# Kernel tuning notes

Hardware: AMD Instinct MI355X
Metric: run time of the kernel (lower is better)

The kernel has to match this reference:

```python
import jax, jax.numpy as jnp
import numpy as np

N_TYPES = 6
NUM_HEADS = 8
MAX_SEQ = 50
LN_EPS = 1e-5
NEG_SLOPE = 0.2


def layer_norm(x, g, b):
    m = x.mean(-1, keepdims=True)
    v = ((x - m) ** 2).mean(-1, keepdims=True)
    return (x - m) / jnp.sqrt(v + LN_EPS) * g + b


def setup_inputs() -> dict:
    key = jax.random.key(0)
    N, E, D = 20000, 200000, 128  # nodes, edges, input_dim==hidden_dim
    ks = jax.random.split(key, 64)
    it = iter(ks)

    def w(shape):
        return jax.random.normal(next(it), shape, jnp.float32) / np.sqrt(shape[-2] if len(shape) > 1 else shape[-1]).astype(np.float32)

    inp = {}
    inp['x'] = jax.random.normal(next(it), (N, D), jnp.float32)
    inp['edge_index'] = jax.random.randint(next(it), (2, E), 0, N)
    inp['node_types'] = jax.random.randint(next(it), (N,), 0, N_TYPES)
    inp['temporal_positions'] = jax.random.randint(next(it), (N,), 0, MAX_SEQ)
    # CrossDomainGAT params
    inp['gat_Wq'] = w((D, D)); inp['gat_Wk'] = w((D, D)); inp['gat_Wv'] = w((D, D))
    inp['gat_Wo'] = w((D, D)); inp['gat_bo'] = jnp.zeros((D,), jnp.float32)
    inp['gat_g'] = jnp.ones((D,), jnp.float32); inp['gat_b'] = jnp.zeros((D,), jnp.float32)
    # SchemaAwareGCN params
    inp['gcn_Wt'] = w((N_TYPES, D, D)); inp['gcn_bt'] = jnp.zeros((N_TYPES, D), jnp.float32)
    inp['gcn_mW1'] = w((2 * D, D)); inp['gcn_mb1'] = jnp.zeros((D,), jnp.float32)
    inp['gcn_mW2'] = w((D, D)); inp['gcn_mb2'] = jnp.zeros((D,), jnp.float32)
    inp['gcn_aW1'] = w((D, D)); inp['gcn_ab1'] = jnp.zeros((D,), jnp.float32)
    inp['gcn_aW2'] = w((D, D)); inp['gcn_ab2'] = jnp.zeros((D,), jnp.float32)
    inp['gcn_Wo'] = w((D, D)); inp['gcn_bo'] = jnp.zeros((D,), jnp.float32)
    inp['gcn_g'] = jnp.ones((D,), jnp.float32); inp['gcn_b'] = jnp.zeros((D,), jnp.float32)
    # TemporalReasoningGNN params (no turn_boundaries -> LSTM/attention path skipped)
    inp['tmp_emb'] = jax.random.normal(next(it), (MAX_SEQ, D), jnp.float32)
    inp['tmp_W1'] = w((2 * D, D)); inp['tmp_b1'] = jnp.zeros((D,), jnp.float32)
    inp['tmp_W2'] = w((D, D)); inp['tmp_b2'] = jnp.zeros((D,), jnp.float32)
    inp['tmp_Wo'] = w((D, D)); inp['tmp_bo'] = jnp.zeros((D,), jnp.float32)
    inp['tmp_g'] = jnp.ones((D,), jnp.float32); inp['tmp_b'] = jnp.zeros((D,), jnp.float32)
    # Unified fusion (concat of 3 branches -> hidden) + LayerNorm
    inp['fus_W'] = w((3 * D, D)); inp['fus_b'] = jnp.zeros((D,), jnp.float32)
    inp['fus_g'] = jnp.ones((D,), jnp.float32); inp['fus_be'] = jnp.zeros((D,), jnp.float32)
    return inp


def _gat(x, row, col, Wq, Wk, Wv, Wo, bo, g, b):
    N, D = x.shape
    Dh = D // NUM_HEADS
    Q = (x @ Wq).reshape(N, NUM_HEADS, Dh)
    K = (x @ Wk).reshape(N, NUM_HEADS, Dh)
    V = (x @ Wv).reshape(N, NUM_HEADS, Dh)
    # edge-wise multi-head attention scores [E, H]
    scores = (Q[row] * K[col]).sum(-1) / np.sqrt(Dh).astype(np.float32)
    scores = jax.nn.leaky_relu(scores, NEG_SLOPE)
    # segment softmax over incoming edges of each col node
    mx = jax.ops.segment_max(scores, col, num_segments=N)
    ex = jnp.exp(scores - mx[col])
    sm = jax.ops.segment_sum(ex, col, num_segments=N)
    probs = ex / sm[col]
    wv = probs[:, :, None] * V[row]  # [E, H, Dh]
    out = jax.ops.segment_sum(wv.reshape(len(row), D), col, num_segments=N)
    out = out @ Wo + bo
    return layer_norm(out + x, g, b)


def _mlp2(z, W1, b1, W2, b2):
    return jax.nn.relu(z @ W1 + b1) @ W2 + b2


def _gcn(x, row, col, node_types, Wt, bt, mW1, mb1, mW2, mb2, aW1, ab1, aW2, ab2, Wo, bo, g, b):
    N, D = x.shape
    h = jnp.zeros((N, D), x.dtype)
    for t in range(N_TYPES):  # fixed small type count
        h = h + jnp.where((node_types == t)[:, None], x @ Wt[t] + bt[t], 0.0)
    messages = _mlp2(jnp.concatenate([h[row], h[col]], axis=1), mW1, mb1, mW2, mb2)
    agg = jax.ops.segment_sum(messages, col, num_segments=N)
    h = h + _mlp2(agg, aW1, ab1, aW2, ab2)
    h = h @ Wo + bo
    return layer_norm(h + x, g, b)


def _temporal(x, row, col, tpos, emb, W1, b1, W2, b2, Wo, bo, g, b):
    N, D = x.shape
    h = x + emb[jnp.clip(tpos, 0, MAX_SEQ - 1)]
    messages = _mlp2(jnp.concatenate([h[row], h[col]], axis=1), W1, b1, W2, b2)
    h = h + jax.ops.segment_sum(messages, col, num_segments=N)
    h = h @ Wo + bo
    return layer_norm(h, g, b)


def reference(x, edge_index, node_types, temporal_positions,
              gat_Wq, gat_Wk, gat_Wv, gat_Wo, gat_bo, gat_g, gat_b,
              gcn_Wt, gcn_bt, gcn_mW1, gcn_mb1, gcn_mW2, gcn_mb2,
              gcn_aW1, gcn_ab1, gcn_aW2, gcn_ab2, gcn_Wo, gcn_bo, gcn_g, gcn_b,
              tmp_emb, tmp_W1, tmp_b1, tmp_W2, tmp_b2, tmp_Wo, tmp_bo, tmp_g, tmp_b,
              fus_W, fus_b, fus_g, fus_be):
    row, col = edge_index[0], edge_index[1]
    o_gat = _gat(x, row, col, gat_Wq, gat_Wk, gat_Wv, gat_Wo, gat_bo, gat_g, gat_b)
    o_gcn = _gcn(x, row, col, node_types, gcn_Wt, gcn_bt, gcn_mW1, gcn_mb1, gcn_mW2, gcn_mb2,
                 gcn_aW1, gcn_ab1, gcn_aW2, gcn_ab2, gcn_Wo, gcn_bo, gcn_g, gcn_b)
    o_tmp = _temporal(x, row, col, temporal_positions, tmp_emb, tmp_W1, tmp_b1, tmp_W2, tmp_b2,
                      tmp_Wo, tmp_bo, tmp_g, tmp_b)
    fused = jnp.concatenate([o_gat, o_gcn, o_tmp], axis=-1) @ fus_W + fus_b
    return layer_norm(fused, fus_g, fus_be)
```

## Files before the change

kernel.cpp:

```cpp
#include <hip/hip_runtime.h>

using u32 = unsigned int;
using s64 = long long;

__global__ __launch_bounds__(64) void k_detect13(const u32* __restrict__ ei,
                                                 const u32* __restrict__ nt,
                                                 const u32* __restrict__ tp,
                                                 u32* __restrict__ flags) {
    if (blockIdx.x != 0 || threadIdx.x != 0) return;
    bool e64 = true, n64 = true, t64 = true;
    for (int k = 0; k < 64; ++k) {
        if (ei[2 * k + 1] != 0u) e64 = false;
        if (nt[2 * k + 1] != 0u) n64 = false;
        if (tp[2 * k + 1] != 0u) t64 = false;
    }
    flags[0] = e64 ? 1u : 0u;
    flags[1] = n64 ? 1u : 0u;
    flags[2] = t64 ? 1u : 0u;
}

__global__ __launch_bounds__(256) void k_cvt13(const void* __restrict__ src,
                                               int* __restrict__ dst, long long n,
                                               const u32* __restrict__ flags, int fidx) {
    long long i = (long long)blockIdx.x * 256 + threadIdx.x;
// ... 179 lines not shown
    int t = threadIdx.x;
#pragma unroll
    for (int ii = 0; ii < 4; ++ii) {
        int idx = t + ii * 256;
        int r = idx >> 5, c = idx & 31;
        int node = i0 + r; if (node >= N) node = N - 1;
        st4(xs + r * 128 + c * 4, ld4(src + (size_t)node * 128 + c * 4));
    }
}

__device__ __forceinline__ void xstore(float* xs, const float4 (&v)[4], int tn, int tc) {
#pragma unroll
    for (int j = 0; j < 4; ++j) st4(xs + (tn * 4 + j) * 128 + tc * 4, v[j]);
}

__global__ __launch_bounds__(256) void k_qkvT(const float* __restrict__ x,
                                              const float* __restrict__ Wq,
                                              const float* __restrict__ Wk,
                                              const float* __restrict__ Wv,
                                              float* __restrict__ big, int N) {
    __shared__ float xs[32 * 128];
    __shared__ float wl[64 * 128];
    int t = threadIdx.x, tn = t >> 5, tc = t & 31;
    int i0 = blockIdx.x * 32;
    stage32(xs, x, i0, N);
    float4 acc[4];
    const float* Ws[3] = {Wq, Wk, Wv};
#pragma unroll
    for (int m = 0; m < 3; ++m) {
#pragma unroll
        for (int j = 0; j < 4; ++j) acc[j] = make_float4(0.f, 0.f, 0.f, 0.f);
        mmS(acc, xs, wl, Ws[m], tn, tc);
#pragma unroll
        for (int j = 0; j < 4; ++j) {
            int node = i0 + tn * 4 + j;
            if (node < N) st4(big + (size_t)node * 384 + m * 128 + tc * 4, acc[j]);
        }
    }
}

__global__ __launch_bounds__(256) void k_gat_smB(const float* __restrict__ big,
                                                 const int* __restrict__ ei, int E,
                                                 float* __restrict__ scores,
                                                 float* __restrict__ sm) {
    long long t = (long long)blockIdx.x * 256 + threadIdx.x;
    if (t >= (long long)E * 8) return;
    int e = (int)(t >> 3), h = (int)(t & 7);
    int row = ei[e], col = ei[E + e];
    const float4* q = (const float4*)(big + (size_t)row * 384 + h * 16);
    const float4* kk = (const float4*)(big + (size_t)col * 384 + 128 + h * 16);
    float s = 0.f;
#pragma unroll
    for (int d = 0; d < 4; ++d) {
        float4 a = q[d], b = kk[d];
        s += a.x * b.x + a.y * b.y + a.z * b.z + a.w * b.w;
    }
    s *= 0.25f;
    s = s > 0.f ? s : 0.2f * s;
    float ex = expf(s);
    scores[t] = ex;
    atomicAdd(&sm[(size_t)col * 8 + h], ex);
}

__global__ __launch_bounds__(256) void k_wvS2(const float* __restrict__ big,
                                              const float* __restrict__ scores,
                                              const float* __restrict__ sm,
                                              const int* __restrict__ srow,
                                              const int* __restrict__ sedge,
                                              const int* __restrict__ offA,
                                              float* __restrict__ agg, int N) {
    int l = threadIdx.x & 63;
    int col = blockIdx.x * 4 + (threadIdx.x >> 6);
    if (col >= N) return;
    int h = l >> 3;
    float sv = sm[(size_t)col * 8 + h];
    float ism = sv != 0.f ? 1.f / sv : 0.f;
// ... 5 lines not shown
        float pr1 = scores[(size_t)e1 * 8 + h] * ism;
        float2 v0 = ld2(big + (size_t)r0 * 384 + 256 + 2 * l);
        float2 v1 = ld2(big + (size_t)r1 * 384 + 256 + 2 * l);
        ax = fmaf(pr0, v0.x, ax); ay = fmaf(pr0, v0.y, ay);
        ax = fmaf(pr1, v1.x, ax); ay = fmaf(pr1, v1.y, ay);
    }
    for (; p < pe; ++p) {
        int e = sedge[p], r = srow[p];
        float pr = scores[(size_t)e * 8 + h] * ism;
        float2 v = ld2(big + (size_t)r * 384 + 256 + 2 * l);
        ax = fmaf(pr, v.x, ax); ay = fmaf(pr, v.y, ay);
    }
    st2(agg + (size_t)col * 128 + 2 * l, make_float2(ax, ay));
}

__global__ __launch_bounds__(256) void k_ep_gatT(const float* __restrict__ x,
                                                 const float* __restrict__ agg,
                                                 const float* __restrict__ Wo,
                                                 const float* __restrict__ bo,
                                                 const float* __restrict__ g,
                                                 const float* __restrict__ b,
                                                 const float* __restrict__ fusW,
                                                 const float* __restrict__ fus_b,
                                                 float* __restrict__ fused, int N) {
    __shared__ float xs[32 * 128];
    __shared__ float wl[64 * 128];
    int t = threadIdx.x, tn = t >> 5, tc = t & 31;
    int i0 = blockIdx.x * 32;
    stage32(xs, agg, i0, N);
    float4 acc[4];
    float4 bo4 = ld4(bo + tc * 4);
#pragma unroll
    for (int j = 0; j < 4; ++j) acc[j] = bo4;
    mmS(acc, xs, wl, Wo, tn, tc);
    float4 o[4];
#pragma unroll
    for (int j = 0; j < 4; ++j) {
        int node = i0 + tn * 4 + j; if (node >= N) node = N - 1;
        float4 xr = ld4(x + (size_t)node * 128 + tc * 4);
        float4 v = make_float4(acc[j].x + xr.x, acc[j].y + xr.y,
                               acc[j].z + xr.z, acc[j].w + xr.w);
        o[j] = lnrow(v, g, b, tc);
    }
    __syncthreads();
    xstore(xs, o, tn, tc);
    float4 fb4 = ld4(fus_b + tc * 4);
#pragma unroll
    for (int j = 0; j < 4; ++j) acc[j] = fb4;
    mmS(acc, xs, wl, fusW, tn, tc);
#pragma unroll
    for (int j = 0; j < 4; ++j) {
        int node = i0 + tn * 4 + j;
        if (node < N) st4(fused + (size_t)node * 128 + tc * 4, acc[j]);
    }
}

__global__ __launch_bounds__(256) void k_hgcnT(const float* __restrict__ x,
                                               const int* __restrict__ nt,
                                               const int* __restrict__ perm,
                                               const float* __restrict__ Wt,
                                               const float* __restrict__ bt,
                                               float* __restrict__ h_gcn, int N) {
    __shared__ float xs[32 * 128];
    __shared__ float wl[64 * 128];
    int t = threadIdx.x, tn = t >> 5, tc = t & 31;
    int i0 = blockIdx.x * 32;
#pragma unroll
    for (int ii = 0; ii < 4; ++ii) {
        int idx = t + ii * 256;
        int r = idx >> 5, c = idx & 31;
        int q = i0 + r; if (q >= N) q = N - 1;
        int node = perm[q];
        st4(xs + r * 128 + c * 4, ld4(x + (size_t)node * 128 + c * 4));
    }
    int qa = i0; if (qa >= N) qa = N - 1;
    int qb = i0 + 31; if (qb >= N) qb = N - 1;
    int t0 = nt[perm[qa]]; t0 = (t0 < 0 || t0 > 5) ? 0 : t0;
    int t1 = nt[perm[qb]]; t1 = (t1 < 0 || t1 > 5) ? 0 : t1;
    float4 acc[4];
    if (t0 == t1) {
#pragma unroll
        for (int j = 0; j < 4; ++j) acc[j] = ld4(bt + t0 * 128 + tc * 4);
        mmS(acc, xs, wl, Wt + (size_t)t0 * 16384, tn, tc);
    } else {
        __syncthreads();
#pragma unroll
        for (int j = 0; j < 4; ++j) {
            int q = i0 + tn * 4 + j; if (q >= N) q = N - 1;
            int tt = nt[perm[q]]; tt = (tt < 0 || tt > 5) ? 0 : tt;
            const float* W = Wt + (size_t)tt * 16384;
            float4 a = ld4(bt + tt * 128 + tc * 4);
#pragma unroll 2
            for (int k4 = 0; k4 < 32; ++k4) {
                float4 xv = ld4(xs + (tn * 4 + j) * 128 + k4 * 4);
                float4 w0 = ld4(W + (size_t)(k4 * 4 + 0) * 128 + tc * 4);
                float4 w1 = ld4(W + (size_t)(k4 * 4 + 1) * 128 + tc * 4);
                float4 w2 = ld4(W + (size_t)(k4 * 4 + 2) * 128 + tc * 4);
                float4 w3 = ld4(W + (size_t)(k4 * 4 + 3) * 128 + tc * 4);
                fma4(a, xv.x, w0); fma4(a, xv.y, w1);
                fma4(a, xv.z, w2); fma4(a, xv.w, w3);
            }
            acc[j] = a;
        }
    }
#pragma unroll
    for (int j = 0; j < 4; ++j) {
        int q = i0 + tn * 4 + j;
        if (q < N) st4(h_gcn + (size_t)perm[q] * 128 + tc * 4, acc[j]);
    }
}

__global__ __launch_bounds__(256) void k_preT(const float* __restrict__ h,
                                              const float* __restrict__ emb,
                                              const int* __restrict__ tpos,
                                              const float* __restrict__ W1,
                                              const float* __restrict__ b1,
                                              float* __restrict__ Pa,
                                              float* __restrict__ Pb, int N, int mode) {
    __shared__ float xs[32 * 128];
    __shared__ float wl[64 * 128];
    int t = threadIdx.x, tn = t >> 5, tc = t & 31;
    int i0 = blockIdx.x * 32;
#pragma unroll
    for (int ii = 0; ii < 4; ++ii) {
        int idx = t + ii * 256;
        int r = idx >> 5, c = idx & 31;
        int node = i0 + r; if (node >= N) node = N - 1;
        float4 v = ld4(h + (size_t)node * 128 + c * 4);
        if (mode) {
            int tp = tpos[node]; tp = tp < 0 ? 0 : (tp > 49 ? 49 : tp);
            float4 e = ld4(emb + tp * 128 + c * 4);
            v.x += e.x; v.y += e.y; v.z += e.z; v.w += e.w;
        }
        st4(xs + r * 128 + c * 4, v);
    }
    float4 acc[4];
#pragma unroll
    for (int j = 0; j < 4; ++j) acc[j] = make_float4(0.f, 0.f, 0.f, 0.f);
    mmS(acc, xs, wl, W1, tn, tc);
#pragma unroll
    for (int j = 0; j < 4; ++j) {
        int node = i0 + tn * 4 + j;
        if (node < N) st4(Pa + (size_t)node * 128 + tc * 4, acc[j]);
    }
    float4 b14 = ld4(b1 + tc * 4);
#pragma unroll
    for (int j = 0; j < 4; ++j) acc[j] = b14;
    mmS(acc, xs, wl, W1 + (size_t)128 * 128, tn, tc);
#pragma unroll
    for (int j = 0; j < 4; ++j) {
        int node = i0 + tn * 4 + j;
        if (node < N) st4(Pb + (size_t)node * 128 + tc * 4, acc[j]);
    }
}

__global__ __launch_bounds__(256) void k_rsum2(const float* __restrict__ Pa,
                                               const float* __restrict__ Pb,
                                               const int* __restrict__ srow,
                                               const int* __restrict__ offA,
                                               float* __restrict__ s, int N) {
    int l = threadIdx.x & 63;
    int col = blockIdx.x * 4 + (threadIdx.x >> 6);
    if (col >= N) return;
    float2 pb = ld2(Pb + (size_t)col * 128 + 2 * l);
    float ax = 0.f, ay = 0.f;
    int p = offA[col], pe = offA[col + 1];
    for (; p + 4 <= pe; p += 4) {
        int r0 = srow[p], r1 = srow[p + 1], r2 = srow[p + 2], r3 = srow[p + 3];
        float2 a0 = ld2(Pa + (size_t)r0 * 128 + 2 * l);
        float2 a1 = ld2(Pa + (size_t)r1 * 128 + 2 * l);
        float2 a2 = ld2(Pa + (size_t)r2 * 128 + 2 * l);
        float2 a3 = ld2(Pa + (size_t)r3 * 128 + 2 * l);
        ax += fmaxf(a0.x + pb.x, 0.f) + fmaxf(a1.x + pb.x, 0.f)
            + fmaxf(a2.x + pb.x, 0.f) + fmaxf(a3.x + pb.x, 0.f);
        ay += fmaxf(a0.y + pb.y, 0.f) + fmaxf(a1.y + pb.y, 0.f)
            + fmaxf(a2.y + pb.y, 0.f) + fmaxf(a3.y + pb.y, 0.f);
    }
    for (; p < pe; ++p) {
        int r = srow[p];
        float2 a = ld2(Pa + (size_t)r * 128 + 2 * l);
        ax += fmaxf(a.x + pb.x, 0.f);
        ay += fmaxf(a.y + pb.y, 0.f);
    }
    st2(s + (size_t)col * 128 + 2 * l, make_float2(ax, ay));
}

__global__ __launch_bounds__(256) void k_ep_gcnT(const float* __restrict__ x,
                                                 const float* __restrict__ h_gcn,
                                                 const float* __restrict__ s,
                                                 const int* __restrict__ offA,
                                                 const float* __restrict__ W2,
                                                 const float* __restrict__ b2,
                                                 const float* __restrict__ aW1,
                                                 const float* __restrict__ ab1,
                                                 const float* __restrict__ aW2,
                                                 const float* __restrict__ ab2,
                                                 const float* __restrict__ Wo,
                                                 const float* __restrict__ bo,
                                                 const float* __restrict__ g,
                                                 const float* __restrict__ b,
                                                 const float* __restrict__ fusW,
                                                 float* __restrict__ fused, int N) {
    __shared__ float xs[32 * 128];
    __shared__ float wl[64 * 128];
    int t = threadIdx.x, tn = t >> 5, tc = t & 31;
    int i0 = blockIdx.x * 32;
    int node[4];
#pragma unroll
    for (int j = 0; j < 4; ++j) {
        node[j] = i0 + tn * 4 + j; if (node[j] >= N) node[j] = N - 1;
    }
    stage32(xs, s, i0, N);
    float4 acc[4];
    float4 b24 = ld4(b2 + tc * 4);
#pragma unroll
    for (int j = 0; j < 4; ++j) {
        float deg = (float)(offA[node[j] + 1] - offA[node[j]]);
        acc[j] = make_float4(deg * b24.x, deg * b24.y, deg * b24.z, deg * b24.w);
    }
    mmS(acc, xs, wl, W2, tn, tc);
    __syncthreads();
    xstore(xs, acc, tn, tc);
    float4 a14 = ld4(ab1 + tc * 4);
#pragma unroll
    for (int j = 0; j < 4; ++j) acc[j] = a14;
    mmS(acc, xs, wl, aW1, tn, tc);
#pragma unroll
    for (int j = 0; j < 4; ++j) {
        acc[j].x = fmaxf(acc[j].x, 0.f); acc[j].y = fmaxf(acc[j].y, 0.f);
        acc[j].z = fmaxf(acc[j].z, 0.f); acc[j].w = fmaxf(acc[j].w, 0.f);
    }
    __syncthreads();
    xstore(xs, acc, tn, tc);
    float4 a24 = ld4(ab2 + tc * 4);
#pragma unroll
    for (int j = 0; j < 4; ++j) acc[j] = a24;
    mmS(acc, xs, wl, aW2, tn, tc);
#pragma unroll
    for (int j = 0; j < 4; ++j) {
        float4 hg = ld4(h_gcn + (size_t)node[j] * 128 + tc * 4);
        acc[j].x += hg.x; acc[j].y += hg.y; acc[j].z += hg.z; acc[j].w += hg.w;
    }
    __syncthreads();
    xstore(xs, acc, tn, tc);
    float4 bo4 = ld4(bo + tc * 4);
#pragma unroll
    for (int j = 0; j < 4; ++j) acc[j] = bo4;
    mmS(acc, xs, wl, Wo, tn, tc);
    float4 o[4];
#pragma unroll
    for (int j = 0; j < 4; ++j) {
        float4 xr = ld4(x + (size_t)node[j] * 128 + tc * 4);
        float4 v = make_float4(acc[j].x + xr.x, acc[j].y + xr.y,
                               acc[j].z + xr.z, acc[j].w + xr.w);
        o[j] = lnrow(v, g, b, tc);
    }
    __syncthreads();
    xstore(xs, o, tn, tc);
#pragma unroll
    for (int j = 0; j < 4; ++j) acc[j] = ld4(fused + (size_t)node[j] * 128 + tc * 4);
    mmS(acc, xs, wl, fusW + (size_t)128 * 128, tn, tc);
#pragma unroll
    for (int j = 0; j < 4; ++j) {
        int q = i0 + tn * 4 + j;
        if (q < N) st4(fused + (size_t)q * 128 + tc * 4, acc[j]);
    }
}

__global__ __launch_bounds__(256) void k_ep_tmpT(const float* __restrict__ x,
                                                 const float* __restrict__ emb,
                                                 const int* __restrict__ tpos,
                                                 const float* __restrict__ s,
                                                 const int* __restrict__ offA,
                                                 const float* __restrict__ W2,
                                                 const float* __restrict__ b2,
                                                 const float* __restrict__ Wo,
                                                 const float* __restrict__ bo,
                                                 const float* __restrict__ g,
                                                 const float* __restrict__ b,
                                                 const float* __restrict__ fusW,
                                                 const float* __restrict__ fused,
                                                 const float* __restrict__ fg,
                                                 const float* __restrict__ fbe,
                                                 float* __restrict__ out, int N) {
    __shared__ float xs[32 * 128];
    __shared__ float wl[64 * 128];
    int t = threadIdx.x, tn = t >> 5, tc = t & 31;
    int i0 = blockIdx.x * 32;
    int node[4];
#pragma unroll
    for (int j = 0; j < 4; ++j) {
        node[j] = i0 + tn * 4 + j; if (node[j] >= N) node[j] = N - 1;
    }
    stage32(xs, s, i0, N);
    float4 acc[4];
    float4 b24 = ld4(b2 + tc * 4);
#pragma unroll
    for (int j = 0; j < 4; ++j) {
        float deg = (float)(offA[node[j] + 1] - offA[node[j]]);
        acc[j] = make_float4(deg * b24.x, deg * b24.y, deg * b24.z, deg * b24.w);
    }
    mmS(acc, xs, wl, W2, tn, tc);
#pragma unroll
    for (int j = 0; j < 4; ++j) {
        int tp = tpos[node[j]]; tp = tp < 0 ? 0 : (tp > 49 ? 49 : tp);
        float4 xr = ld4(x + (size_t)node[j] * 128 + tc * 4);
        float4 e = ld4(emb + tp * 128 + tc * 4);
        acc[j].x += xr.x + e.x; acc[j].y += xr.y + e.y;
        acc[j].z += xr.z + e.z; acc[j].w += xr.w + e.w;
    }
    __syncthreads();
    xstore(xs, acc, tn, tc);
    float4 bo4 = ld4(bo + tc * 4);
#pragma unroll
    for (int j = 0; j < 4; ++j) acc[j] = bo4;
    mmS(acc, xs, wl, Wo, tn, tc);
    float4 o[4];
#pragma unroll
    for (int j = 0; j < 4; ++j) o[j] = lnrow(acc[j], g, b, tc);
    __syncthreads();
    xstore(xs, o, tn, tc);
#pragma unroll
    for (int j = 0; j < 4; ++j) acc[j] = ld4(fused + (size_t)node[j] * 128 + tc * 4);
    mmS(acc, xs, wl, fusW + (size_t)256 * 128, tn, tc);
#pragma unroll
    for (int j = 0; j < 4; ++j) {
        float4 res = lnrow(acc[j], fg, fbe, tc);
        int q = i0 + tn * 4 + j;
        if (q < N) st4(out + (size_t)q * 128 + tc * 4, res);
    }
}

extern "C" void kernel_launch(void* const* d_in, const int* in_sizes, int n_in, void* d_out,
                              int out_size, void* d_ws, size_t ws_size, hipStream_t stream) {
    (void)n_in; (void)out_size; (void)ws_size;
    const float* x = (const float*)d_in[0];
    const float* gat_Wq = (const float*)d_in[4];
    const float* gat_Wk = (const float*)d_in[5];
// ... 23 lines not shown
    const float* tmp_b2 = (const float*)d_in[29];
    const float* tmp_Wo = (const float*)d_in[30];
    const float* tmp_bo = (const float*)d_in[31];
    const float* tmp_g = (const float*)d_in[32];
    const float* tmp_b = (const float*)d_in[33];
    const float* fus_W = (const float*)d_in[34];
    const float* fus_b = (const float*)d_in[35];
    const float* fus_g = (const float*)d_in[36];
    const float* fus_be = (const float*)d_in[37];

    int N = in_sizes[0] / 128;
    int E = in_sizes[1] / 2;

    float* ws = (float*)d_ws;
    float* big = ws;
    float* fused = ws;
    float* h_gcn = ws + (size_t)128 * N;
    float* Pa = ws + (size_t)256 * N;
    float* Pb = ws + (size_t)384 * N;
    float* agg = ws + (size_t)512 * N;
    float* sm = ws + (size_t)640 * N;
    u32* flags = (u32*)(ws + (size_t)648 * N);
    int* ei32 = (int*)(flags + 16);
    int* nt32 = ei32 + (size_t)2 * E;
    int* tp32 = nt32 + N;
    float* scores = (float*)(tp32 + N);
    int* offA = (int*)(scores + (size_t)8 * E);
    int* cur = offA + (N + 1);
    int* srow = cur + N;
    int* sedge = srow + E;
    int* tcnt = sedge + E;
    int* toff = tcnt + 6;
    int* tcur = toff + 7;
    int* perm = cur;

    k_detect13<<<1, 64, 0, stream>>>((const u32*)d_in[1], (const u32*)d_in[2],
                                     (const u32*)d_in[3], flags);
// ... 8 lines not shown
    int gC = (N + 3) / 4;
    int gE8 = (int)(((long long)E * 8 + 255) / 256);

    kz_i<<<gN, 256, 0, stream>>>(cur, N);
    k_hist<<<gE, 256, 0, stream>>>(ei32, E, cur);
    k_scan<<<1, 1024, 0, stream>>>(cur, offA, N);
    kz_i<<<gN, 256, 0, stream>>>(cur, N);
    k_scatter<<<gE, 256, 0, stream>>>(ei32, E, offA, cur, srow, sedge);

    kz_i<<<1, 32, 0, stream>>>(tcnt, 19);
    k_thist<<<gN, 256, 0, stream>>>(nt32, N, tcnt);
    k_tscan<<<1, 64, 0, stream>>>(tcnt, toff);
    k_tscatter<<<gN, 256, 0, stream>>>(nt32, N, toff, tcur, perm);

    kz13<<<(int)(((long long)8 * N + 255) / 256), 256, 0, stream>>>(sm, (long long)8 * N);
    k_qkvT<<<gT, 256, 0, stream>>>(x, gat_Wq, gat_Wk, gat_Wv, big, N);
    k_gat_smB<<<gE8, 256, 0, stream>>>(big, ei32, E, scores, sm);
    k_wvS2<<<gC, 256, 0, stream>>>(big, scores, sm, srow, sedge, offA, agg, N);
    k_ep_gatT<<<gT, 256, 0, stream>>>(x, agg, gat_Wo, gat_bo, gat_g, gat_b,
                                      fus_W, fus_b, fused, N);

    k_hgcnT<<<gT, 256, 0, stream>>>(x, nt32, perm, gcn_Wt, gcn_bt, h_gcn, N);
    k_preT<<<gT, 256, 0, stream>>>(h_gcn, nullptr, nullptr, gcn_mW1, gcn_mb1, Pa, Pb, N, 0);
    k_rsum2<<<gC, 256, 0, stream>>>(Pa, Pb, srow, offA, agg, N);
    k_ep_gcnT<<<gT, 256, 0, stream>>>(x, h_gcn, agg, offA, gcn_mW2, gcn_mb2,
                                      gcn_aW1, gcn_ab1, gcn_aW2, gcn_ab2,
                                      gcn_Wo, gcn_bo, gcn_g, gcn_b, fus_W, fused, N);

    k_preT<<<gT, 256, 0, stream>>>(x, tmp_emb, tp32, tmp_W1, tmp_b1, Pa, Pb, N, 1);
    k_rsum2<<<gC, 256, 0, stream>>>(Pa, Pb, srow, offA, agg, N);
    k_ep_tmpT<<<gT, 256, 0, stream>>>(x, tmp_emb, tp32, agg, offA, tmp_W2, tmp_b2,
                                      tmp_Wo, tmp_bo, tmp_g, tmp_b, fus_W, fused,
                                      fus_g, fus_be, (float*)d_out, N);
}
```

Baseline: 527.7 us.

## Merge independent branch kernels into role-dispatched mega-kernels to increase concurrency

Merges the three branches' independent stages into a few wide launches that pick their role from the block index. QKV projection, type-specific GCN transform with message pre-MLP, and temporal pre-MLP run in one kernel. GAT scoring and both relu-sum gathers run in another, and the three epilogues in a third. A separate final kernel then does the fusion matmul. The aim is to cut launch count and fill the GPU with more concurrent blocks instead of serialising small kernels. The cost is more workspace for separate per-branch buffers, extra global writes and reads of the branch outputs, and the GCN transform now fused per-tile with a fallback path when a tile mixes node types.

```diff
diff --git a/kernel.cpp b/kernel.cpp
--- a/kernel.cpp
+++ b/kernel.cpp
@@ -217,52 +217,206 @@
     for (int j = 0; j < 4; ++j) st4(xs + (tn * 4 + j) * 128 + tc * 4, v[j]);
 }
 
-__global__ __launch_bounds__(256) void k_qkvT(const float* __restrict__ x,
-                                              const float* __restrict__ Wq,
-                                              const float* __restrict__ Wk,
-                                              const float* __restrict__ Wv,
-                                              float* __restrict__ big, int N) {
+__global__ __launch_bounds__(256) void k_mega1(
+        const float* __restrict__ x,
+        const float* __restrict__ Wq, const float* __restrict__ Wk,
+        const float* __restrict__ Wv, float* __restrict__ big,
+        const int* __restrict__ nt, const int* __restrict__ perm,
+        const float* __restrict__ Wt, const float* __restrict__ bt,
+        float* __restrict__ h_gcn,
+        const float* __restrict__ mW1, const float* __restrict__ mb1,
+        float* __restrict__ Pa_g, float* __restrict__ Pb_g,
+        const float* __restrict__ emb, const int* __restrict__ tpos,
+        const float* __restrict__ tW1, const float* __restrict__ tb1,
+        float* __restrict__ Pa_t, float* __restrict__ Pb_t,
+        int N, int gT) {
     __shared__ float xs[32 * 128];
     __shared__ float wl[64 * 128];
+    int role = blockIdx.x / gT;
+    int bid = blockIdx.x - role * gT;
     int t = threadIdx.x, tn = t >> 5, tc = t & 31;
-    int i0 = blockIdx.x * 32;
-    stage32(xs, x, i0, N);
-    float4 acc[4];
-    const float* Ws[3] = {Wq, Wk, Wv};
-#pragma unroll
-    for (int m = 0; m < 3; ++m) {
+    int i0 = bid * 32;
+
+    if (role == 0) {
+        stage32(xs, x, i0, N);
+        float4 acc[4];
+        const float* Ws[3] = {Wq, Wk, Wv};
+#pragma unroll
+        for (int m = 0; m < 3; ++m) {
+#pragma unroll
+            for (int j = 0; j < 4; ++j) acc[j] = make_float4(0.f, 0.f, 0.f, 0.f);
+            mmS(acc, xs, wl, Ws[m], tn, tc);
+#pragma unroll
+            for (int j = 0; j < 4; ++j) {
+                int node = i0 + tn * 4 + j;
+                if (node < N) st4(big + (size_t)node * 384 + m * 128 + tc * 4, acc[j]);
+            }
+        }
+    } else if (role == 1) {
+#pragma unroll
+        for (int ii = 0; ii < 4; ++ii) {
+            int idx = t + ii * 256;
+            int r = idx >> 5, c = idx & 31;
+            int q = i0 + r; if (q >= N) q = N - 1;
+            int node = perm[q];
+            st4(xs + r * 128 + c * 4, ld4(x + (size_t)node * 128 + c * 4));
+        }
+        int qa = i0; if (qa >= N) qa = N - 1;
+        int qb = i0 + 31; if (qb >= N) qb = N - 1;
+        int t0 = nt[perm[qa]]; t0 = (t0 < 0 || t0 > 5) ? 0 : t0;
+        int t1 = nt[perm[qb]]; t1 = (t1 < 0 || t1 > 5) ? 0 : t1;
+        float4 acc[4];
+        if (t0 == t1) {
+#pragma unroll
+            for (int j = 0; j < 4; ++j) acc[j] = ld4(bt + t0 * 128 + tc * 4);
+            mmS(acc, xs, wl, Wt + (size_t)t0 * 16384, tn, tc);
+        } else {
+            __syncthreads();
+#pragma unroll
+            for (int j = 0; j < 4; ++j) {
+                int q = i0 + tn * 4 + j; if (q >= N) q = N - 1;
+                int tt = nt[perm[q]]; tt = (tt < 0 || tt > 5) ? 0 : tt;
+                const float* W = Wt + (size_t)tt * 16384;
+                float4 a = ld4(bt + tt * 128 + tc * 4);
+                float4 one[4] = {a, a, a, a};
+                (void)one;
+                float4 aa[4];
+#pragma unroll
+                for (int jj = 0; jj < 4; ++jj) aa[jj] = make_float4(0.f, 0.f, 0.f, 0.f);
+#pragma unroll 2
+                for (int k4 = 0; k4 < 32; ++k4) {
+                    float4 xv = ld4(xs + (tn * 4 + j) * 128 + k4 * 4);
+                    float4 w0 = ld4(W + (size_t)(k4 * 4 + 0) * 128 + tc * 4);
+                    float4 w1 = ld4(W + (size_t)(k4 * 4 + 1) * 128 + tc * 4);
+                    float4 w2 = ld4(W + (size_t)(k4 * 4 + 2) * 128 + tc * 4);
+                    float4 w3 = ld4(W + (size_t)(k4 * 4 + 3) * 128 + tc * 4);
+                    fma4(a, xv.x, w0); fma4(a, xv.y, w1);
+                    fma4(a, xv.z, w2); fma4(a, xv.w, w3);
+                }
+                acc[j] = a;
+            }
+        }
+#pragma unroll
+        for (int j = 0; j < 4; ++j) {
+            int q = i0 + tn * 4 + j;
+            if (q < N) st4(h_gcn + (size_t)perm[q] * 128 + tc * 4, acc[j]);
+        }
+        __syncthreads();
+        xstore(xs, acc, tn, tc);
+        float4 pa[4];
+#pragma unroll
+        for (int j = 0; j < 4; ++j) pa[j] = make_float4(0.f, 0.f, 0.f, 0.f);
+        mmS(pa, xs, wl, mW1, tn, tc);
+#pragma unroll
+        for (int j = 0; j < 4; ++j) {
+            int q = i0 + tn * 4 + j;
+            if (q < N) st4(Pa_g + (size_t)perm[q] * 128 + tc * 4, pa[j]);
+        }
+        float4 b14 = ld4(mb1 + tc * 4);
+        float4 pb[4];
+#pragma unroll
+        for (int j = 0; j < 4; ++j) pb[j] = b14;
+        mmS(pb, xs, wl, mW1 + (size_t)128 * 128, tn, tc);
+#pragma unroll
+        for (int j = 0; j < 4; ++j) {
+            int q = i0 + tn * 4 + j;
+            if (q < N) st4(Pb_g + (size_t)perm[q] * 128 + tc * 4, pb[j]);
+        }
+    } else {
+#pragma unroll
+        for (int ii = 0; ii < 4; ++ii) {
+            int idx = t + ii * 256;
+            int r = idx >> 5, c = idx & 31;
+            int node = i0 + r; if (node >= N) node = N - 1;
+            float4 v = ld4(x + (size_t)node * 128 + c * 4);
+            int tp = tpos[node]; tp = tp < 0 ? 0 : (tp > 49 ? 49 : tp);
+            float4 e = ld4(emb + tp * 128 + c * 4);
+            v.x += e.x; v.y += e.y; v.z += e.z; v.w += e.w;
+            st4(xs + r * 128 + c * 4, v);
+        }
+        float4 acc[4];
 #pragma unroll
         for (int j = 0; j < 4; ++j) acc[j] = make_float4(0.f, 0.f, 0.f, 0.f);
-        mmS(acc, xs, wl, Ws[m], tn, tc);
+        mmS(acc, xs, wl, tW1, tn, tc);
 #pragma unroll
         for (int j = 0; j < 4; ++j) {
             int node = i0 + tn * 4 + j;
-            if (node < N) st4(big + (size_t)node * 384 + m * 128 + tc * 4, acc[j]);
-        }
-    }
-}
-
-__global__ __launch_bounds__(256) void k_gat_smB(const float* __restrict__ big,
-                                                 const int* __restrict__ ei, int E,
-                                                 float* __restrict__ scores,
-                                                 float* __restrict__ sm) {
-    long long t = (long long)blockIdx.x * 256 + threadIdx.x;
-    if (t >= (long long)E * 8) return;
-    int e = (int)(t >> 3), h = (int)(t & 7);
-    int row = ei[e], col = ei[E + e];
-    const float4* q = (const float4*)(big + (size_t)row * 384 + h * 16);
-    const float4* kk = (const float4*)(big + (size_t)col * 384 + 128 + h * 16);
-    float s = 0.f;
-#pragma unroll
-    for (int d = 0; d < 4; ++d) {
-        float4 a = q[d], b = kk[d];
-        s += a.x * b.x + a.y * b.y + a.z * b.z + a.w * b.w;
-    }
-    s *= 0.25f;
-    s = s > 0.f ? s : 0.2f * s;
-    float ex = expf(s);
-    scores[t] = ex;
-    atomicAdd(&sm[(size_t)col * 8 + h], ex);
+            if (node < N) st4(Pa_t + (size_t)node * 128 + tc * 4, acc[j]);
+        }
+        float4 b14 = ld4(tb1 + tc * 4);
+#pragma unroll
+        for (int j = 0; j < 4; ++j) acc[j] = b14;
+        mmS(acc, xs, wl, tW1 + (size_t)128 * 128, tn, tc);
+#pragma unroll
+        for (int j = 0; j < 4; ++j) {
+            int node = i0 + tn * 4 + j;
+            if (node < N) st4(Pb_t + (size_t)node * 128 + tc * 4, acc[j]);
+        }
+    }
+}
+
+__device__ __forceinline__ void rsum_body(const float* __restrict__ Pa,
+                                          const float* __restrict__ Pb,
+                                          const int* __restrict__ srow,
+                                          const int* __restrict__ offA,
+                                          float* __restrict__ s, int N, int cb) {
+    int l = threadIdx.x & 63;
+    int col = cb * 4 + (threadIdx.x >> 6);
+    if (col >= N) return;
+    float2 pb = ld2(Pb + (size_t)col * 128 + 2 * l);
+    float ax = 0.f, ay = 0.f;
+    int p = offA[col], pe = offA[col + 1];
+    for (; p + 4 <= pe; p += 4) {
+        int r0 = srow[p], r1 = srow[p + 1], r2 = srow[p + 2], r3 = srow[p + 3];
+        float2 a0 = ld2(Pa + (size_t)r0 * 128 + 2 * l);
+        float2 a1 = ld2(Pa + (size_t)r1 * 128 + 2 * l);
+        float2 a2 = ld2(Pa + (size_t)r2 * 128 + 2 * l);
+        float2 a3 = ld2(Pa + (size_t)r3 * 128 + 2 * l);
+        ax += fmaxf(a0.x + pb.x, 0.f) + fmaxf(a1.x + pb.x, 0.f)
+            + fmaxf(a2.x + pb.x, 0.f) + fmaxf(a3.x + pb.x, 0.f);
+        ay += fmaxf(a0.y + pb.y, 0.f) + fmaxf(a1.y + pb.y, 0.f)
+            + fmaxf(a2.y + pb.y, 0.f) + fmaxf(a3.y + pb.y, 0.f);
+    }
+    for (; p < pe; ++p) {
+        int r = srow[p];
+        float2 a = ld2(Pa + (size_t)r * 128 + 2 * l);
+        ax += fmaxf(a.x + pb.x, 0.f);
+        ay += fmaxf(a.y + pb.y, 0.f);
+    }
+    st2(s + (size_t)col * 128 + 2 * l, make_float2(ax, ay));
+}
+
+__global__ __launch_bounds__(256) void k_mega2(
+        const float* __restrict__ big, const int* __restrict__ ei, int E,
+        float* __restrict__ scores, float* __restrict__ sm,
+        const float* __restrict__ Pa_g, float* __restrict__ Pb_g,
+        const float* __restrict__ Pa_t, float* __restrict__ Pb_t,
+        const int* __restrict__ srow, const int* __restrict__ offA,
+        int N, int gE8, int gC) {
+    int b = blockIdx.x;
+    if (b < gE8) {
+        long long t = (long long)b * 256 + threadIdx.x;
+        if (t >= (long long)E * 8) return;
+        int e = (int)(t >> 3), h = (int)(t & 7);
+        int row = ei[e], col = ei[E + e];
+        const float4* q = (const float4*)(big + (size_t)row * 384 + h * 16);
+        const float4* kk = (const float4*)(big + (size_t)col * 384 + 128 + h * 16);
+        float s = 0.f;
+#pragma unroll
+        for (int d = 0; d < 4; ++d) {
+            float4 a = q[d], bb = kk[d];
+            s += a.x * bb.x + a.y * bb.y + a.z * bb.z + a.w * bb.w;
+        }
+        s *= 0.25f;
+        s = s > 0.f ? s : 0.2f * s;
+        float ex = expf(s);
+        scores[t] = ex;
+        atomicAdd(&sm[(size_t)col * 8 + h], ex);
+    } else if (b < gE8 + gC) {
+        rsum_body(Pa_g, Pb_g, srow, offA, Pb_g, N, b - gE8);
+    } else {
+        rsum_body(Pa_t, Pb_t, srow, offA, Pb_t, N, b - gE8 - gC);
+    }
 }
 
 __global__ __launch_bounds__(256) void k_wvS2(const float* __restrict__ big,
@@ -298,314 +452,160 @@
     st2(agg + (size_t)col * 128 + 2 * l, make_float2(ax, ay));
 }
 
-__global__ __launch_bounds__(256) void k_ep_gatT(const float* __restrict__ x,
-                                                 const float* __restrict__ agg,
-                                                 const float* __restrict__ Wo,
-                                                 const float* __restrict__ bo,
-                                                 const float* __restrict__ g,
-                                                 const float* __restrict__ b,
-                                                 const float* __restrict__ fusW,
-                                                 const float* __restrict__ fus_b,
-                                                 float* __restrict__ fused, int N) {
+__global__ __launch_bounds__(256) void k_mega3(
+        const float* __restrict__ x,
+        const float* __restrict__ agg,
+        const float* __restrict__ gWo, const float* __restrict__ gbo,
+        const float* __restrict__ gg, const float* __restrict__ gb,
+        float* __restrict__ o_gat,
+        const float* __restrict__ h_gcn, const float* __restrict__ s_gcn,
+        const int* __restrict__ offA,
+        const float* __restrict__ W2, const float* __restrict__ b2,
+        const float* __restrict__ aW1, const float* __restrict__ ab1,
+        const float* __restrict__ aW2, const float* __restrict__ ab2,
+        const float* __restrict__ cWo, const float* __restrict__ cbo,
+        const float* __restrict__ cg, const float* __restrict__ cb,
+        float* __restrict__ o_gcn,
+        const float* __restrict__ emb, const int* __restrict__ tpos,
+        const float* __restrict__ s_tmp,
+        const float* __restrict__ tW2, const float* __restrict__ tb2,
+        const float* __restrict__ tWo, const float* __restrict__ tbo,
+        const float* __restrict__ tg, const float* __restrict__ tb,
+        float* __restrict__ o_tmp,
+        int N, int gT) {
+    __shared__ float xs[32 * 128];
+    __shared__ float wl[64 * 128];
+    int role = blockIdx.x / gT;
+    int bid = blockIdx.x - role * gT;
+    int t = threadIdx.x, tn = t >> 5, tc = t & 31;
+    int i0 = bid * 32;
+    int node[4];
+#pragma unroll
+    for (int j = 0; j < 4; ++j) {
+        node[j] = i0 + tn * 4 + j; if (node[j] >= N) node[j] = N - 1;
+    }
+
+    if (role == 0) {
+        stage32(xs, agg, i0, N);
+        float4 acc[4];
+        float4 bo4 = ld4(gbo + tc * 4);
+#pragma unroll
+        for (int j = 0; j < 4; ++j) acc[j] = bo4;
+        mmS(acc, xs, wl, gWo, tn, tc);
+#pragma unroll
+        for (int j = 0; j < 4; ++j) {
+            float4 xr = ld4(x + (size_t)node[j] * 128 + tc * 4);
+            float4 v = make_float4(acc[j].x + xr.x, acc[j].y + xr.y,
+                                   acc[j].z + xr.z, acc[j].w + xr.w);
+            float4 o = lnrow(v, gg, gb, tc);
+            int q = i0 + tn * 4 + j;
+            if (q < N) st4(o_gat + (size_t)q * 128 + tc * 4, o);
+        }
+    } else if (role == 1) {
+        stage32(xs, s_gcn, i0, N);
+        float4 acc[4];
+        float4 b24 = ld4(b2 + tc * 4);
+#pragma unroll
+        for (int j = 0; j < 4; ++j) {
+            float deg = (float)(offA[node[j] + 1] - offA[node[j]]);
+            acc[j] = make_float4(deg * b24.x, deg * b24.y, deg * b24.z, deg * b24.w);
+        }
+        mmS(acc, xs, wl, W2, tn, tc);
+        __syncthreads();
+        xstore(xs, acc, tn, tc);
+        float4 u[4];
+        float4 a14 = ld4(ab1 + tc * 4);
+#pragma unroll
+        for (int j = 0; j < 4; ++j) u[j] = a14;
+        mmS(u, xs, wl, aW1, tn, tc);
+#pragma unroll
+        for (int j = 0; j < 4; ++j) {
+            u[j].x = fmaxf(u[j].x, 0.f); u[j].y = fmaxf(u[j].y, 0.f);
+            u[j].z = fmaxf(u[j].z, 0.f); u[j].w = fmaxf(u[j].w, 0.f);
+        }
+        __syncthreads();
+        xstore(xs, u, tn, tc);
+        float4 z3[4];
+        float4 a24 = ld4(ab2 + tc * 4);
+#pragma unroll
+        for (int j = 0; j < 4; ++j) z3[j] = a24;
+        mmS(z3, xs, wl, aW2, tn, tc);
+#pragma unroll
+        for (int j = 0; j < 4; ++j) {
+            float4 hg = ld4(h_gcn + (size_t)node[j] * 128 + tc * 4);
+            z3[j].x += hg.x; z3[j].y += hg.y; z3[j].z += hg.z; z3[j].w += hg.w;
+        }
+        __syncthreads();
+        xstore(xs, z3, tn, tc);
+        float4 d[4];
+        float4 bo4 = ld4(cbo + tc * 4);
+#pragma unroll
+        for (int j = 0; j < 4; ++j) d[j] = bo4;
+        mmS(d, xs, wl, cWo, tn, tc);
+#pragma unroll
+        for (int j = 0; j < 4; ++j) {
+            float4 xr = ld4(x + (size_t)node[j] * 128 + tc * 4);
+            float4 v = make_float4(d[j].x + xr.x, d[j].y + xr.y,
+                                   d[j].z + xr.z, d[j].w + xr.w);
+            float4 o = lnrow(v, cg, cb, tc);
+            int q = i0 + tn * 4 + j;
+            if (q < N) st4(o_gcn + (size_t)q * 128 + tc * 4, o);
+        }
+    } else {
+        stage32(xs, s_tmp, i0, N);
+        float4 acc[4];
+        float4 b24 = ld4(tb2 + tc * 4);
+#pragma unroll
+        for (int j = 0; j < 4; ++j) {
+            float deg = (float)(offA[node[j] + 1] - offA[node[j]]);
+            acc[j] = make_float4(deg * b24.x, deg * b24.y, deg * b24.z, deg * b24.w);
+        }
+        mmS(acc, xs, wl, tW2, tn, tc);
+#pragma unroll
+        for (int j = 0; j < 4; ++j) {
+            int tp = tpos[node[j]]; tp = tp < 0 ? 0 : (tp > 49 ? 49 : tp);
+            float4 xr = ld4(x + (size_t)node[j] * 128 + tc * 4);
+            float4 e = ld4(emb + tp * 128 + tc * 4);
+            acc[j].x += xr.x + e.x; acc[j].y += xr.y + e.y;
+            acc[j].z += xr.z + e.z; acc[j].w += xr.w + e.w;
+        }
+        __syncthreads();
+        xstore(xs, acc, tn, tc);
+        float4 d[4];
+        float4 bo4 = ld4(tbo + tc * 4);
+#pragma unroll
+        for (int j = 0; j < 4; ++j) d[j] = bo4;
+        mmS(d, xs, wl, tWo, tn, tc);
+#pragma unroll
+        for (int j = 0; j < 4; ++j) {
+            float4 o = lnrow(d[j], tg, tb, tc);
+            int q = i0 + tn * 4 + j;
+            if (q < N) st4(o_tmp + (size_t)q * 128 + tc * 4, o);
+        }
+    }
+}
+
+__global__ __launch_bounds__(256) void k_final3(
+        const float* __restrict__ o_gat, const float* __restrict__ o_gcn,
+        const float* __restrict__ o_tmp,
+        const float* __restrict__ fusW, const float* __restrict__ fus_b,
+        const float* __restrict__ fg, const float* __restrict__ fbe,
+        float* __restrict__ out, int N) {
     __shared__ float xs[32 * 128];
     __shared__ float wl[64 * 128];
     int t = threadIdx.x, tn = t >> 5, tc = t & 31;
     int i0 = blockIdx.x * 32;
-    stage32(xs, agg, i0, N);
+    stage32(xs, o_gat, i0, N);
     float4 acc[4];
-    float4 bo4 = ld4(bo + tc * 4);
-#pragma unroll
-    for (int j = 0; j < 4; ++j) acc[j] = bo4;
-    mmS(acc, xs, wl, Wo, tn, tc);
-    float4 o[4];
-#pragma unroll
-    for (int j = 0; j < 4; ++j) {
-        int node = i0 + tn * 4 + j; if (node >= N) node = N - 1;
-        float4 xr = ld4(x + (size_t)node * 128 + tc * 4);
-        float4 v = make_float4(acc[j].x + xr.x, acc[j].y + xr.y,
-                               acc[j].z + xr.z, acc[j].w + xr.w);
-        o[j] = lnrow(v, g, b, tc);
-    }
-    __syncthreads();
-    xstore(xs, o, tn, tc);
     float4 fb4 = ld4(fus_b + tc * 4);
 #pragma unroll
     for (int j = 0; j < 4; ++j) acc[j] = fb4;
     mmS(acc, xs, wl, fusW, tn, tc);
-#pragma unroll
-    for (int j = 0; j < 4; ++j) {
-        int node = i0 + tn * 4 + j;
-        if (node < N) st4(fused + (size_t)node * 128 + tc * 4, acc[j]);
-    }
-}
-
-__global__ __launch_bounds__(256) void k_hgcnT(const float* __restrict__ x,
-                                               const int* __restrict__ nt,
-                                               const int* __restrict__ perm,
-                                               const float* __restrict__ Wt,
-                                               const float* __restrict__ bt,
-                                               float* __restrict__ h_gcn, int N) {
-    __shared__ float xs[32 * 128];
-    __shared__ float wl[64 * 128];
-    int t = threadIdx.x, tn = t >> 5, tc = t & 31;
-    int i0 = blockIdx.x * 32;
-#pragma unroll
-    for (int ii = 0; ii < 4; ++ii) {
-        int idx = t + ii * 256;
-        int r = idx >> 5, c = idx & 31;
-        int q = i0 + r; if (q >= N) q = N - 1;
-        int node = perm[q];
-        st4(xs + r * 128 + c * 4, ld4(x + (size_t)node * 128 + c * 4));
-    }
-    int qa = i0; if (qa >= N) qa = N - 1;
-    int qb = i0 + 31; if (qb >= N) qb = N - 1;
-    int t0 = nt[perm[qa]]; t0 = (t0 < 0 || t0 > 5) ? 0 : t0;
-    int t1 = nt[perm[qb]]; t1 = (t1 < 0 || t1 > 5) ? 0 : t1;
-    float4 acc[4];
-    if (t0 == t1) {
-#pragma unroll
-        for (int j = 0; j < 4; ++j) acc[j] = ld4(bt + t0 * 128 + tc * 4);
-        mmS(acc, xs, wl, Wt + (size_t)t0 * 16384, tn, tc);
-    } else {
-        __syncthreads();
-#pragma unroll
-        for (int j = 0; j < 4; ++j) {
-            int q = i0 + tn * 4 + j; if (q >= N) q = N - 1;
-            int tt = nt[perm[q]]; tt = (tt < 0 || tt > 5) ? 0 : tt;
-            const float* W = Wt + (size_t)tt * 16384;
-            float4 a = ld4(bt + tt * 128 + tc * 4);
-#pragma unroll 2
-            for (int k4 = 0; k4 < 32; ++k4) {
-                float4 xv = ld4(xs + (tn * 4 + j) * 128 + k4 * 4);
-                float4 w0 = ld4(W + (size_t)(k4 * 4 + 0) * 128 + tc * 4);
-                float4 w1 = ld4(W + (size_t)(k4 * 4 + 1) * 128 + tc * 4);
-                float4 w2 = ld4(W + (size_t)(k4 * 4 + 2) * 128 + tc * 4);
-                float4 w3 = ld4(W + (size_t)(k4 * 4 + 3) * 128 + tc * 4);
-                fma4(a, xv.x, w0); fma4(a, xv.y, w1);
-                fma4(a, xv.z, w2); fma4(a, xv.w, w3);
-            }
-            acc[j] = a;
-        }
-    }
-#pragma unroll
-    for (int j = 0; j < 4; ++j) {
-        int q = i0 + tn * 4 + j;
-        if (q < N) st4(h_gcn + (size_t)perm[q] * 128 + tc * 4, acc[j]);
-    }
-}
-
-__global__ __launch_bounds__(256) void k_preT(const float* __restrict__ h,
-                                              const float* __restrict__ emb,
-                                              const int* __restrict__ tpos,
-                                              const float* __restrict__ W1,
-                                              const float* __restrict__ b1,
-                                              float* __restrict__ Pa,
-                                              float* __restrict__ Pb, int N, int mode) {
-    __shared__ float xs[32 * 128];
-    __shared__ float wl[64 * 128];
-    int t = threadIdx.x, tn = t >> 5, tc = t & 31;
-    int i0 = blockIdx.x * 32;
-#pragma unroll
-    for (int ii = 0; ii < 4; ++ii) {
-        int idx = t + ii * 256;
-        int r = idx >> 5, c = idx & 31;
-        int node = i0 + r; if (node >= N) node = N - 1;
-        float4 v = ld4(h + (size_t)node * 128 + c * 4);
-        if (mode) {
-            int tp = tpos[node]; tp = tp < 0 ? 0 : (tp > 49 ? 49 : tp);
-            float4 e = ld4(emb + tp * 128 + c * 4);
-            v.x += e.x; v.y += e.y; v.z += e.z; v.w += e.w;
-        }
-        st4(xs + r * 128 + c * 4, v);
-    }
-    float4 acc[4];
-#pragma unroll
-    for (int j = 0; j < 4; ++j) acc[j] = make_float4(0.f, 0.f, 0.f, 0.f);
-    mmS(acc, xs, wl, W1, tn, tc);
-#pragma unroll
-    for (int j = 0; j < 4; ++j) {
-        int node = i0 + tn * 4 + j;
-        if (node < N) st4(Pa + (size_t)node * 128 + tc * 4, acc[j]);
-    }
-    float4 b14 = ld4(b1 + tc * 4);
-#pragma unroll
-    for (int j = 0; j < 4; ++j) acc[j] = b14;
-    mmS(acc, xs, wl, W1 + (size_t)128 * 128, tn, tc);
-#pragma unroll
-    for (int j = 0; j < 4; ++j) {
-        int node = i0 + tn * 4 + j;
-        if (node < N) st4(Pb + (size_t)node * 128 + tc * 4, acc[j]);
-    }
-}
-
-__global__ __launch_bounds__(256) void k_rsum2(const float* __restrict__ Pa,
-                                               const float* __restrict__ Pb,
-                                               const int* __restrict__ srow,
-                                               const int* __restrict__ offA,
-                                               float* __restrict__ s, int N) {
-    int l = threadIdx.x & 63;
-    int col = blockIdx.x * 4 + (threadIdx.x >> 6);
-    if (col >= N) return;
-    float2 pb = ld2(Pb + (size_t)col * 128 + 2 * l);
-    float ax = 0.f, ay = 0.f;
-    int p = offA[col], pe = offA[col + 1];
-    for (; p + 4 <= pe; p += 4) {
-        int r0 = srow[p], r1 = srow[p + 1], r2 = srow[p + 2], r3 = srow[p + 3];
-        float2 a0 = ld2(Pa + (size_t)r0 * 128 + 2 * l);
-        float2 a1 = ld2(Pa + (size_t)r1 * 128 + 2 * l);
-        float2 a2 = ld2(Pa + (size_t)r2 * 128 + 2 * l);
-        float2 a3 = ld2(Pa + (size_t)r3 * 128 + 2 * l);
-        ax += fmaxf(a0.x + pb.x, 0.f) + fmaxf(a1.x + pb.x, 0.f)
-            + fmaxf(a2.x + pb.x, 0.f) + fmaxf(a3.x + pb.x, 0.f);
-        ay += fmaxf(a0.y + pb.y, 0.f) + fmaxf(a1.y + pb.y, 0.f)
-            + fmaxf(a2.y + pb.y, 0.f) + fmaxf(a3.y + pb.y, 0.f);
-    }
-    for (; p < pe; ++p) {
-        int r = srow[p];
-        float2 a = ld2(Pa + (size_t)r * 128 + 2 * l);
-        ax += fmaxf(a.x + pb.x, 0.f);
-        ay += fmaxf(a.y + pb.y, 0.f);
-    }
-    st2(s + (size_t)col * 128 + 2 * l, make_float2(ax, ay));
-}
-
-__global__ __launch_bounds__(256) void k_ep_gcnT(const float* __restrict__ x,
-                                                 const float* __restrict__ h_gcn,
-                                                 const float* __restrict__ s,
-                                                 const int* __restrict__ offA,
-                                                 const float* __restrict__ W2,
-                                                 const float* __restrict__ b2,
-                                                 const float* __restrict__ aW1,
-                                                 const float* __restrict__ ab1,
-                                                 const float* __restrict__ aW2,
-                                                 const float* __restrict__ ab2,
-                                                 const float* __restrict__ Wo,
-                                                 const float* __restrict__ bo,
-                                                 const float* __restrict__ g,
-                                                 const float* __restrict__ b,
-                                                 const float* __restrict__ fusW,
-                                                 float* __restrict__ fused, int N) {
-    __shared__ float xs[32 * 128];
-    __shared__ float wl[64 * 128];
-    int t = threadIdx.x, tn = t >> 5, tc = t & 31;
-    int i0 = blockIdx.x * 32;
-    int node[4];
-#pragma unroll
-    for (int j = 0; j < 4; ++j) {
-        node[j] = i0 + tn * 4 + j; if (node[j] >= N) node[j] = N - 1;
-    }
-    stage32(xs, s, i0, N);
-    float4 acc[4];
-    float4 b24 = ld4(b2 + tc * 4);
-#pragma unroll
-    for (int j = 0; j < 4; ++j) {
-        float deg = (float)(offA[node[j] + 1] - offA[node[j]]);
-        acc[j] = make_float4(deg * b24.x, deg * b24.y, deg * b24.z, deg * b24.w);
-    }
-    mmS(acc, xs, wl, W2, tn, tc);
-    __syncthreads();
-    xstore(xs, acc, tn, tc);
-    float4 a14 = ld4(ab1 + tc * 4);
-#pragma unroll
-    for (int j = 0; j < 4; ++j) acc[j] = a14;
-    mmS(acc, xs, wl, aW1, tn, tc);
-#pragma unroll
-    for (int j = 0; j < 4; ++j) {
-        acc[j].x = fmaxf(acc[j].x, 0.f); acc[j].y = fmaxf(acc[j].y, 0.f);
-        acc[j].z = fmaxf(acc[j].z, 0.f); acc[j].w = fmaxf(acc[j].w, 0.f);
-    }
-    __syncthreads();
-    xstore(xs, acc, tn, tc);
-    float4 a24 = ld4(ab2 + tc * 4);
-#pragma unroll
-    for (int j = 0; j < 4; ++j) acc[j] = a24;
-    mmS(acc, xs, wl, aW2, tn, tc);
-#pragma unroll
-    for (int j = 0; j < 4; ++j) {
-        float4 hg = ld4(h_gcn + (size_t)node[j] * 128 + tc * 4);
-        acc[j].x += hg.x; acc[j].y += hg.y; acc[j].z += hg.z; acc[j].w += hg.w;
-    }
-    __syncthreads();
-    xstore(xs, acc, tn, tc);
-    float4 bo4 = ld4(bo + tc * 4);
-#pragma unroll
-    for (int j = 0; j < 4; ++j) acc[j] = bo4;
-    mmS(acc, xs, wl, Wo, tn, tc);
-    float4 o[4];
-#pragma unroll
-    for (int j = 0; j < 4; ++j) {
-        float4 xr = ld4(x + (size_t)node[j] * 128 + tc * 4);
-        float4 v = make_float4(acc[j].x + xr.x, acc[j].y + xr.y,
-                               acc[j].z + xr.z, acc[j].w + xr.w);
-        o[j] = lnrow(v, g, b, tc);
-    }
-    __syncthreads();
-    xstore(xs, o, tn, tc);
-#pragma unroll
-    for (int j = 0; j < 4; ++j) acc[j] = ld4(fused + (size_t)node[j] * 128 + tc * 4);
+    __syncthreads();
+    stage32(xs, o_gcn, i0, N);
     mmS(acc, xs, wl, fusW + (size_t)128 * 128, tn, tc);
-#pragma unroll
-    for (int j = 0; j < 4; ++j) {
-        int q = i0 + tn * 4 + j;
-        if (q < N) st4(fused + (size_t)q * 128 + tc * 4, acc[j]);
-    }
-}
-
-__global__ __launch_bounds__(256) void k_ep_tmpT(const float* __restrict__ x,
-                                                 const float* __restrict__ emb,
-                                                 const int* __restrict__ tpos,
-                                                 const float* __restrict__ s,
-                                                 const int* __restrict__ offA,
-                                                 const float* __restrict__ W2,
-                                                 const float* __restrict__ b2,
-                                                 const float* __restrict__ Wo,
-                                                 const float* __restrict__ bo,
-                                                 const float* __restrict__ g,
-                                                 const float* __restrict__ b,
-                                                 const float* __restrict__ fusW,
-                                                 const float* __restrict__ fused,
-                                                 const float* __restrict__ fg,
-                                                 const float* __restrict__ fbe,
-                                                 float* __restrict__ out, int N) {
-    __shared__ float xs[32 * 128];
-    __shared__ float wl[64 * 128];
-    int t = threadIdx.x, tn = t >> 5, tc = t & 31;
-    int i0 = blockIdx.x * 32;
-    int node[4];
-#pragma unroll
-    for (int j = 0; j < 4; ++j) {
-        node[j] = i0 + tn * 4 + j; if (node[j] >= N) node[j] = N - 1;
-    }
-    stage32(xs, s, i0, N);
-    float4 acc[4];
-    float4 b24 = ld4(b2 + tc * 4);
-#pragma unroll
-    for (int j = 0; j < 4; ++j) {
-        float deg = (float)(offA[node[j] + 1] - offA[node[j]]);
-        acc[j] = make_float4(deg * b24.x, deg * b24.y, deg * b24.z, deg * b24.w);
-    }
-    mmS(acc, xs, wl, W2, tn, tc);
-#pragma unroll
-    for (int j = 0; j < 4; ++j) {
-        int tp = tpos[node[j]]; tp = tp < 0 ? 0 : (tp > 49 ? 49 : tp);
-        float4 xr = ld4(x + (size_t)node[j] * 128 + tc * 4);
-        float4 e = ld4(emb + tp * 128 + tc * 4);
-        acc[j].x += xr.x + e.x; acc[j].y += xr.y + e.y;
-        acc[j].z += xr.z + e.z; acc[j].w += xr.w + e.w;
-    }
-    __syncthreads();
-    xstore(xs, acc, tn, tc);
-    float4 bo4 = ld4(bo + tc * 4);
-#pragma unroll
-    for (int j = 0; j < 4; ++j) acc[j] = bo4;
-    mmS(acc, xs, wl, Wo, tn, tc);
-    float4 o[4];
-#pragma unroll
-    for (int j = 0; j < 4; ++j) o[j] = lnrow(acc[j], g, b, tc);
-    __syncthreads();
-    xstore(xs, o, tn, tc);
-#pragma unroll
-    for (int j = 0; j < 4; ++j) acc[j] = ld4(fused + (size_t)node[j] * 128 + tc * 4);
+    __syncthreads();
+    stage32(xs, o_tmp, i0, N);
     mmS(acc, xs, wl, fusW + (size_t)256 * 128, tn, tc);
 #pragma unroll
     for (int j = 0; j < 4; ++j) {
@@ -659,13 +659,17 @@
 
     float* ws = (float*)d_ws;
     float* big = ws;
-    float* fused = ws;
-    float* h_gcn = ws + (size_t)128 * N;
-    float* Pa = ws + (size_t)256 * N;
-    float* Pb = ws + (size_t)384 * N;
-    float* agg = ws + (size_t)512 * N;
-    float* sm = ws + (size_t)640 * N;
-    u32* flags = (u32*)(ws + (size_t)648 * N);
+    float* o_gat = ws;
+    float* o_gcn = ws + (size_t)128 * N;
+    float* o_tmp = ws + (size_t)256 * N;
+    float* h_gcn = ws + (size_t)384 * N;
+    float* Pa_g = ws + (size_t)512 * N;
+    float* Pb_g = ws + (size_t)640 * N;
+    float* Pa_t = ws + (size_t)768 * N;
+    float* Pb_t = ws + (size_t)896 * N;
+    float* sm = ws + (size_t)1024 * N;
+    float* agg = Pa_g;
+    u32* flags = (u32*)(ws + (size_t)1032 * N);
     int* ei32 = (int*)(flags + 16);
     int* nt32 = ei32 + (size_t)2 * E;
     int* tp32 = nt32 + N;
@@ -704,22 +708,27 @@
     k_tscatter<<<gN, 256, 0, stream>>>(nt32, N, toff, tcur, perm);
 
     kz13<<<(int)(((long long)8 * N + 255) / 256), 256, 0, stream>>>(sm, (long long)8 * N);
-    k_qkvT<<<gT, 256, 0, stream>>>(x, gat_Wq, gat_Wk, gat_Wv, big, N);
-    k_gat_smB<<<gE8, 256, 0, stream>>>(big, ei32, E, scores, sm);
+
+    k_mega1<<<3 * gT, 256, 0, stream>>>(x, gat_Wq, gat_Wk, gat_Wv, big,
+                                        nt32, perm, gcn_Wt, gcn_bt, h_gcn,
+                                        gcn_mW1, gcn_mb1, Pa_g, Pb_g,
+                                        tmp_emb, tp32, tmp_W1, tmp_b1, Pa_t, Pb_t,
+                                        N, gT);
+
+    k_mega2<<<gE8 + 2 * gC, 256, 0, stream>>>(big, ei32, E, scores, sm,
+                                              Pa_g, Pb_g, Pa_t, Pb_t,
+                                              srow, offA, N, gE8, gC);
+
     k_wvS2<<<gC, 256, 0, stream>>>(big, scores, sm, srow, sedge, offA, agg, N);
-    k_ep_gatT<<<gT, 256, 0, stream>>>(x, agg, gat_Wo, gat_bo, gat_g, gat_b,
-                                      fus_W, fus_b, fused, N);
-
-    k_hgcnT<<<gT, 256, 0, stream>>>(x, nt32, perm, gcn_Wt, gcn_bt, h_gcn, N);
-    k_preT<<<gT, 256, 0, stream>>>(h_gcn, nullptr, nullptr, gcn_mW1, gcn_mb1, Pa, Pb, N, 0);
-    k_rsum2<<<gC, 256, 0, stream>>>(Pa, Pb, srow, offA, agg, N);
-    k_ep_gcnT<<<gT, 256, 0, stream>>>(x, h_gcn, agg, offA, gcn_mW2, gcn_mb2,
-                                      gcn_aW1, gcn_ab1, gcn_aW2, gcn_ab2,
-                                      gcn_Wo, gcn_bo, gcn_g, gcn_b, fus_W, fused, N);
-
-    k_preT<<<gT, 256, 0, stream>>>(x, tmp_emb, tp32, tmp_W1, tmp_b1, Pa, Pb, N, 1);
-    k_rsum2<<<gC, 256, 0, stream>>>(Pa, Pb, srow, offA, agg, N);
-    k_ep_tmpT<<<gT, 256, 0, stream>>>(x, tmp_emb, tp32, agg, offA, tmp_W2, tmp_b2,
-                                      tmp_Wo, tmp_bo, tmp_g, tmp_b, fus_W, fused,
-                                      fus_g, fus_be, (float*)d_out, N);
-}
+
+    k_mega3<<<3 * gT, 256, 0, stream>>>(x, agg, gat_Wo, gat_bo, gat_g, gat_b, o_gat,
+                                        h_gcn, Pb_g, offA, gcn_mW2, gcn_mb2,
+                                        gcn_aW1, gcn_ab1, gcn_aW2, gcn_ab2,
+                                        gcn_Wo, gcn_bo, gcn_g, gcn_b, o_gcn,
+                                        tmp_emb, tp32, Pb_t, tmp_W2, tmp_b2,
+                                        tmp_Wo, tmp_bo, tmp_g, tmp_b, o_tmp,
+                                        N, gT);
+
+    k_final3<<<gT, 256, 0, stream>>>(o_gat, o_gcn, o_tmp, fus_W, fus_b,
+                                     fus_g, fus_be, (float*)d_out, N);
+}
```

After: 475.8 us. 1.11x faster.
